# Optimization experiments

Hardware: AMD Instinct MI355X
Metric: run time of the kernel (lower is better)

The kernel has to match this reference:

```python
import jax, jax.numpy as jnp
import numpy as np
from jax import lax

DN = ('NCHW', 'OIHW', 'NCHW')

def conv3x3(x, w):
    return lax.conv_general_dilated(x, w, (1, 1), 'SAME', dimension_numbers=DN)

def conv1x1(x, w, b):
    # w: [O, C], x: [B, C, H, W]
    return jnp.einsum('oc,bchw->bohw', w, x) + b[None, :, None, None]

def bn_relu(x, p):
    # p: [2, C] -> (scale, shift), eval-mode folded BatchNorm + ReLU
    return jax.nn.relu(x * p[0][None, :, None, None] + p[1][None, :, None, None])

def pam(y, Wb, bb, Wc, bc, Wd, bd, alpha):
    B, C, H, W = y.shape
    n = H * W
    b_ = conv1x1(y, Wb, bb).reshape(B, -1, n)   # [B, C/8, N]
    c_ = conv1x1(y, Wc, bc).reshape(B, -1, n)   # [B, C/8, N]
    d_ = conv1x1(y, Wd, bd).reshape(B, C, n)    # [B, C, N]
    energy = jnp.einsum('bkn,bkm->bnm', b_, c_)  # [B, N, N]
    attn = jax.nn.softmax(energy, axis=-1)
    feat = jnp.einsum('bcm,bnm->bcn', d_, attn).reshape(B, C, H, W)
    return alpha[0] * feat + y

def cam(y, beta):
    B, C, H, W = y.shape
    xf = y.reshape(B, C, H * W)
    energy = jnp.einsum('bcn,bdn->bcd', xf, xf)  # [B, C, C]
    energy = jnp.max(energy, axis=-1, keepdims=True) - energy
    attn = jax.nn.softmax(energy, axis=-1)
    feat = jnp.einsum('bcd,bdn->bcn', attn, xf).reshape(B, C, H, W)
    return beta[0] * feat + y

def reference(x, Wp1, bnp1, Wc1, bnc1, Wb, bb, Wc, bc, Wd, bd, alpha, beta,
              Wp2, bnp2, Wc2, bnc2, Wout, bout, Wp3, bp3, Wc3, bc3):
    feat_p = bn_relu(conv3x3(x, Wp1), bnp1)
    feat_p = pam(feat_p, Wb, bb, Wc, bc, Wd, bd, alpha)
    feat_p = bn_relu(conv3x3(feat_p, Wp2), bnp2)

    feat_c = bn_relu(conv3x3(x, Wc1), bnc1)
    feat_c = cam(feat_c, beta)
    feat_c = bn_relu(conv3x3(feat_c, Wc2), bnc2)

    fusion = feat_p + feat_c
    out_main = jax.nn.sigmoid(conv1x1(fusion, Wout, bout))
    out_p = jax.nn.sigmoid(conv1x1(feat_p, Wp3, bp3))
    out_c = jax.nn.sigmoid(conv1x1(feat_c, Wc3, bc3))
    return (out_main, out_p, out_c)

def setup_inputs() -> dict:
    key = jax.random.key(0)
    ks = jax.random.split(key, 24)
    Cin, Ci, Ck, NC = 512, 128, 16, 19
    B, H, W = 8, 64, 64
    s = lambda k, shape, scale=0.05: jax.random.normal(k, shape, jnp.float32) * scale
    return {
        'x': jax.random.normal(ks[0], (B, Cin, H, W), jnp.float32),
        'Wp1': s(ks[1], (Ci, Cin, 3, 3)), 'bnp1': jnp.stack([jnp.ones(Ci), jnp.zeros(Ci)]),
        'Wc1': s(ks[2], (Ci, Cin, 3, 3)), 'bnc1': jnp.stack([jnp.ones(Ci), jnp.zeros(Ci)]),
        'Wb': s(ks[3], (Ck, Ci)), 'bb': s(ks[4], (Ck,)),
        'Wc': s(ks[5], (Ck, Ci)), 'bc': s(ks[6], (Ck,)),
        'Wd': s(ks[7], (Ci, Ci)), 'bd': s(ks[8], (Ci,)),
        'alpha': jax.random.normal(ks[9], (1,), jnp.float32) * 0.5,
        'beta': jax.random.normal(ks[10], (1,), jnp.float32) * 0.5,
        'Wp2': s(ks[11], (Ci, Ci, 3, 3)), 'bnp2': jnp.stack([jnp.ones(Ci), jnp.zeros(Ci)]),
        'Wc2': s(ks[12], (Ci, Ci, 3, 3)), 'bnc2': jnp.stack([jnp.ones(Ci), jnp.zeros(Ci)]),
        'Wout': s(ks[13], (NC, Ci)), 'bout': s(ks[14], (NC,)),
        'Wp3': s(ks[15], (NC, Ci)), 'bp3': s(ks[16], (NC,)),
        'Wc3': s(ks[17], (NC, Ci)), 'bc3': s(ks[18], (NC,)),
    }
```

## Files before the change

### kernel.cpp

```cpp
#include <hip/hip_runtime.h>
#include <math.h>


typedef __attribute__((ext_vector_type(8)))  short short8;
typedef __attribute__((ext_vector_type(16))) float f32x16;

__device__ inline unsigned short f2bf(float f) {
    union { float f; unsigned u; } v; v.f = f;
    unsigned r = v.u + 0x7fffu + ((v.u >> 16) & 1u);
    return (unsigned short)(r >> 16);
}
__device__ inline float bf2f(unsigned short h) {
    union { unsigned u; float f; } v; v.u = ((unsigned)h) << 16;
    return v.f;
}

__global__ __launch_bounds__(256) void wpack_kernel(
    const float* __restrict__ W, unsigned short* __restrict__ wp, int Cin, int total)
{
    int idx = blockIdx.x * 256 + threadIdx.x;
    if (idx >= total) return;
    int chunk = idx / 18432;
    int rem   = idx - chunk * 18432;
    int tap   = rem >> 11;
    int rem2  = rem & 2047;
    int co    = rem2 >> 4;
    int ci    = rem2 & 15;
    int cin   = (chunk << 4) + ci;
    wp[idx] = f2bf(W[((size_t)co * Cin + cin) * 9 + tap]);
}

__global__ __launch_bounds__(256) void wpack_split_kernel(
    const float* __restrict__ W, unsigned short* __restrict__ wph,
    unsigned short* __restrict__ wpl, int Cin, int total)
{
    int idx = blockIdx.x * 256 + threadIdx.x;
    if (idx >= total) return;
    int chunk = idx / 18432;
    int rem   = idx - chunk * 18432;
    int tap   = rem >> 11;
    int rem2  = rem & 2047;
    int co    = rem2 >> 4;
    int ci    = rem2 & 15;
    int cin   = (chunk << 4) + ci;
    float w = W[((size_t)co * Cin + cin) * 9 + tap];
    unsigned short hi = f2bf(w);
    wph[idx] = hi;
    wpl[idx] = f2bf(w - bf2f(hi));
}

__global__ __launch_bounds__(256) void x_split_kernel(
    const float* __restrict__ x, unsigned short* __restrict__ xh,
    unsigned short* __restrict__ xl)
{
    const int ch = blockIdx.x;
    const int b  = blockIdx.y;
    const int t  = threadIdx.x;
    for (int seg = 0; seg < 16; ++seg) {
        const int n = (seg << 8) + t;
        unsigned short uh[16], ul[16];
#pragma unroll
        for (int c = 0; c < 16; ++c) {
            float f = x[(((size_t)b * 512 + (ch << 4) + c) << 12) + n];
            unsigned short hi = f2bf(f);
            uh[c] = hi;
            ul[c] = f2bf(f - bf2f(hi));
        }
        size_t dst = ((((size_t)b * 32 + ch) << 12) + n) << 4;
        *(uint4*)(xh + dst)     = ((uint4*)uh)[0];
        *(uint4*)(xh + dst + 8) = ((uint4*)uh)[1];
        *(uint4*)(xl + dst)     = ((uint4*)ul)[0];
        *(uint4*)(xl + dst + 8) = ((uint4*)ul)[1];
    }
}

__global__ __launch_bounds__(256) void conv3x3_mfma(
    const unsigned short* __restrict__ xb, int Cin,
    const unsigned short* __restrict__ wpack, const float* __restrict__ bn,
    float* __restrict__ out_f32)
{
    const int t   = threadIdx.x;
    const int w   = t >> 6;
    const int wy  = w >> 1;
    const int wx  = w & 1;
    const int ln  = t & 63;
    const int l31 = ln & 31;
    const int g   = ln >> 5;
    const int y0  = blockIdx.x << 1;
    const int co0 = blockIdx.y << 6;
    const int b   = blockIdx.z;
    const int nc16 = Cin >> 4;

    __shared__ __align__(16) unsigned short Xl[4 * 66 * 16];
    __shared__ __align__(16) unsigned short Wl[9 * 64 * 16];

    if (t < 8) {
        int r = t >> 1, xc = (t & 1) * 65;
        uint4 z = {0, 0, 0, 0};
        *(uint4*)&Xl[(r * 66 + xc) * 16 + 0] = z;
        *(uint4*)&Xl[(r * 66 + xc) * 16 + 8] = z;
    }

    const f32x16 zero = {0,0,0,0,0,0,0,0,0,0,0,0,0,0,0,0};
    f32x16 acc0 = zero, acc1 = zero;

    for (int ch = 0; ch < nc16; ++ch) {
#pragma unroll
        for (int it = 0; it < 2; ++it) {
            int idx = t + (it << 8);
            int r = idx >> 7, u = idx & 127;
            int gy = y0 - 1 + r;
            uint4 val = {0, 0, 0, 0};
            if ((unsigned)gy < 64u)
                val = *(const uint4*)(xb + ((((size_t)(b * nc16 + ch)) << 12) + (gy << 6)) * 16 + (u << 3));
            *(uint4*)&Xl[(r * 66 + 1) * 16 + (u << 3)] = val;
        }
        {
            const uint4* wsrc = (const uint4*)wpack;
            const int base = ch * 2304 + (co0 << 1);
            for (int idx = t; idx < 1152; idx += 256)
                ((uint4*)Wl)[idx] = wsrc[base + ((idx >> 7) << 8) + (idx & 127)];
        }
        __syncthreads();

#pragma unroll 3
        for (int tap = 0; tap < 9; ++tap) {
            const int dy = tap / 3, dx = tap - dy * 3;
            short8 a = *(const short8*)&Wl[((tap << 6) + (wy << 5) + l31) * 16 + (g << 3)];
            const int row = wx + dy;
            short8 b0 = *(const short8*)&Xl[(row * 66 + l31 + dx) * 16 + (g << 3)];
            short8 b1 = *(const short8*)&Xl[(row * 66 + l31 + 32 + dx) * 16 + (g << 3)];
            acc0 = __builtin_amdgcn_mfma_f32_32x32x16_bf16(a, b0, acc0, 0, 0, 0);
            acc1 = __builtin_amdgcn_mfma_f32_32x32x16_bf16(a, b1, acc1, 0, 0, 0);
        }
        __syncthreads();
    }

    const int y = y0 + wx;
#pragma unroll
    for (int j = 0; j < 2; j++) {
        const f32x16 a = j ? acc1 : acc0;
#pragma unroll
        for (int r = 0; r < 16; r++) {
            int co = co0 + (wy << 5) + (r & 3) + ((r >> 2) << 3) + (g << 2);
            int x  = (j << 5) + l31;
            float v = fmaf(a[r], bn[co], bn[128 + co]);
            v = v > 0.f ? v : 0.f;
            out_f32[(((size_t)b * 128 + co) << 12) + (y << 6) + x] = v;
        }
    }
}

__global__ __launch_bounds__(256) void conv3x3_mfma_hilo(
    const unsigned short* __restrict__ xbh, const unsigned short* __restrict__ xbl,
    int Cin, const unsigned short* __restrict__ wph, const unsigned short* __restrict__ wpl,
    const float* __restrict__ bn, float* __restrict__ out_f32,
    unsigned short* __restrict__ outh, unsigned short* __restrict__ outl)
{
    const int t   = threadIdx.x;
    const int w   = t >> 6;
    const int wy  = w >> 1;
    const int wx  = w & 1;
    const int ln  = t & 63;
    const int l31 = ln & 31;
    const int g   = ln >> 5;
    const int y0  = blockIdx.x << 1;
    const int co0 = blockIdx.y << 6;
    const int b   = blockIdx.z;
    const int nc16 = Cin >> 4;

    __shared__ __align__(16) unsigned short Xh[4 * 66 * 16];
    __shared__ __align__(16) unsigned short Xo[4 * 66 * 16];
    __shared__ __align__(16) unsigned short Wh[9 * 64 * 16];
    __shared__ __align__(16) unsigned short Wo[9 * 64 * 16];

    if (t < 8) {
        int r = t >> 1, xc = (t & 1) * 65;
        uint4 z = {0, 0, 0, 0};
        *(uint4*)&Xh[(r * 66 + xc) * 16 + 0] = z;
        *(uint4*)&Xh[(r * 66 + xc) * 16 + 8] = z;
        *(uint4*)&Xo[(r * 66 + xc) * 16 + 0] = z;
        *(uint4*)&Xo[(r * 66 + xc) * 16 + 8] = z;
    }

    const f32x16 zero = {0,0,0,0,0,0,0,0,0,0,0,0,0,0,0,0};
    f32x16 acc0 = zero, acc1 = zero;

    for (int ch = 0; ch < nc16; ++ch) {
#pragma unroll
        for (int it = 0; it < 2; ++it) {
            int idx = t + (it << 8);
            int r = idx >> 7, u = idx & 127;
            int gy = y0 - 1 + r;
            uint4 vh = {0, 0, 0, 0}, vl = {0, 0, 0, 0};
            if ((unsigned)gy < 64u) {
                size_t o = ((((size_t)(b * nc16 + ch)) << 12) + (gy << 6)) * 16 + (u << 3);
                vh = *(const uint4*)(xbh + o);
                vl = *(const uint4*)(xbl + o);
            }
            *(uint4*)&Xh[(r * 66 + 1) * 16 + (u << 3)] = vh;
            *(uint4*)&Xo[(r * 66 + 1) * 16 + (u << 3)] = vl;
        }
        {
            const uint4* sh = (const uint4*)wph;
            const uint4* sl = (const uint4*)wpl;
            const int base = ch * 2304 + (co0 << 1);
            for (int idx = t; idx < 1152; idx += 256) {
                int o = base + ((idx >> 7) << 8) + (idx & 127);
                ((uint4*)Wh)[idx] = sh[o];
                ((uint4*)Wo)[idx] = sl[o];
            }
        }
        __syncthreads();

#pragma unroll 1
        for (int tap = 0; tap < 9; ++tap) {
            const int dy = tap / 3, dx = tap - dy * 3;
            const int wi = ((tap << 6) + (wy << 5) + l31) * 16 + (g << 3);
            const int row = wx + dy;
            const int xi0 = (row * 66 + l31 + dx) * 16 + (g << 3);
            const int xi1 = (row * 66 + l31 + 32 + dx) * 16 + (g << 3);
            short8 ah = *(const short8*)&Wh[wi];
            short8 al = *(const short8*)&Wo[wi];
            short8 b0h = *(const short8*)&Xh[xi0];
            short8 b1h = *(const short8*)&Xh[xi1];
            short8 b0l = *(const short8*)&Xo[xi0];
            short8 b1l = *(const short8*)&Xo[xi1];
            acc0 = __builtin_amdgcn_mfma_f32_32x32x16_bf16(ah, b0h, acc0, 0, 0, 0);
            acc1 = __builtin_amdgcn_mfma_f32_32x32x16_bf16(ah, b1h, acc1, 0, 0, 0);
            acc0 = __builtin_amdgcn_mfma_f32_32x32x16_bf16(ah, b0l, acc0, 0, 0, 0);
            acc1 = __builtin_amdgcn_mfma_f32_32x32x16_bf16(ah, b1l, acc1, 0, 0, 0);
            acc0 = __builtin_amdgcn_mfma_f32_32x32x16_bf16(al, b0h, acc0, 0, 0, 0);
            acc1 = __builtin_amdgcn_mfma_f32_32x32x16_bf16(al, b1h, acc1, 0, 0, 0);
        }
        __syncthreads();
    }

    const int y = y0 + wx;
#pragma unroll
    for (int j = 0; j < 2; j++) {
        const f32x16 a = j ? acc1 : acc0;
#pragma unroll
        for (int r = 0; r < 16; r++) {
            int co = co0 + (wy << 5) + (r & 3) + ((r >> 2) << 3) + (g << 2);
            int x  = (j << 5) + l31;
            float v = fmaf(a[r], bn[co], bn[128 + co]);
            v = v > 0.f ? v : 0.f;
            size_t o = (((size_t)b * 128 + co) << 12) + (y << 6) + x;
            if (out_f32) out_f32[o] = v;
            if (outh) {
                unsigned short hi = f2bf(v);
                outh[o] = hi;
                outl[o] = f2bf(v - bf2f(hi));
            }
        }
    }
}

__global__ __launch_bounds__(256) void cam_energy_mfma(
    const unsigned short* __restrict__ bh, const unsigned short* __restrict__ bl,
    float* __restrict__ egy_part)
{
    const int t   = threadIdx.x;
    const int w   = t >> 6;
    const int ln  = t & 63;
    const int l31 = ln & 31;
    const int g   = ln >> 5;
    const int i0  = (blockIdx.x >> 2) << 5;
    const int j0  = (blockIdx.x & 3) << 5;
    const int nseg = blockIdx.y;
    const int b   = blockIdx.z;

    __shared__ float red[4][64][17];

    const f32x16 zero = {0,0,0,0,0,0,0,0,0,0,0,0,0,0,0,0};
    f32x16 acc = zero;
    const int nb = (nseg << 9) + (w << 7) + (g << 3);
    const size_t ri = ((size_t)b * 128 + i0 + l31) << 12;
    const size_t rj = ((size_t)b * 128 + j0 + l31) << 12;

#pragma unroll
    for (int c = 0; c < 8; c++) {
        const int n0 = nb + (c << 4);
        short8 ah  = *(const short8*)(bh + ri + n0);
        short8 al  = *(const short8*)(bl + ri + n0);
        short8 bhf = *(const short8*)(bh + rj + n0);
        short8 blf = *(const short8*)(bl + rj + n0);
        acc = __builtin_amdgcn_mfma_f32_32x32x16_bf16(ah, bhf, acc, 0, 0, 0);
        acc = __builtin_amdgcn_mfma_f32_32x32x16_bf16(ah, blf, acc, 0, 0, 0);
        acc = __builtin_amdgcn_mfma_f32_32x32x16_bf16(al, bhf, acc, 0, 0, 0);
    }
#pragma unroll
    for (int r = 0; r < 16; r++) red[w][ln][r] = acc[r];
    __syncthreads();

    const int lane = t & 63;
    const int rq   = t >> 6;
    float* base = egy_part + (((size_t)(nseg * 8 + b)) << 14);
#pragma unroll
    for (int e = 0; e < 4; e++) {
        const int reg = (rq << 2) + e;
        float v = red[0][lane][reg] + red[1][lane][reg]
                + red[2][lane][reg] + red[3][lane][reg];
        const int i = i0 + (reg & 3) + ((reg >> 2) << 3) + ((lane >> 5) << 2);
        base[i * 128 + j0 + (lane & 31)] = v;
    }
}

__global__ __launch_bounds__(256) void cam_softmax_fused(
    const float* __restrict__ egy_part, float* __restrict__ egy)
{
    const int b   = blockIdx.x;
    const int rg  = blockIdx.y;
    const int t   = threadIdx.x;
    const int row = (rg << 4) + (t >> 4);
    const int jg  = t & 15;

    float e[8];
#pragma unroll
    for (int jj = 0; jj < 8; jj++) e[jj] = 0.f;
    for (int seg = 0; seg < 8; seg++) {
        const float* p = egy_part + (((size_t)(seg * 8 + b)) << 14) + row * 128 + (jg << 3);
#pragma unroll
        for (int jj = 0; jj < 8; jj++) e[jj] += p[jj];
    }
    float mn = e[0];
#pragma unroll
    for (int jj = 1; jj < 8; jj++) mn = fminf(mn, e[jj]);
#pragma unroll
    for (int k = 1; k < 16; k <<= 1) mn = fminf(mn, __shfl_xor(mn, k));
    float s = 0.f;
#pragma unroll
    for (int jj = 0; jj < 8; jj++) { float p = __expf(mn - e[jj]); e[jj] = p; s += p; }
#pragma unroll
    for (int k = 1; k < 16; k <<= 1) s += __shfl_xor(s, k);
    const float inv = 1.f / s;
    float* orow = egy + ((size_t)b << 14) + row * 128 + (jg << 3);
#pragma unroll
    for (int jj = 0; jj < 8; jj++) orow[jj] = e[jj] * inv;
}

__global__ __launch_bounds__(256) void pam_qk_1x1(
    const float* __restrict__ A, const float* __restrict__ Wb, const float* __restrict__ bb,
    const float* __restrict__ Wc, const float* __restrict__ bc,
    unsigned short* __restrict__ qt, unsigned short* __restrict__ kt)
{
    __shared__ float wl[2 * 16 * 128];
    __shared__ float bl[32];
    const int t = threadIdx.x;
    const int n = (blockIdx.x << 8) + t;
    const int b = blockIdx.y;
    for (int idx = t; idx < 2048; idx += 256) { wl[idx] = Wb[idx]; wl[2048 + idx] = Wc[idx]; }
    if (t < 16) { bl[t] = bb[t]; bl[16 + t] = bc[t]; }
    __syncthreads();
    float ab[16], ac[16];
#pragma unroll
    for (int k = 0; k < 16; k++) { ab[k] = 0.f; ac[k] = 0.f; }
    for (int chn = 0; chn < 128; ++chn) {
        float a = A[(((size_t)b * 128 + chn) << 12) + n];
#pragma unroll
        for (int k = 0; k < 16; k++) {
            ab[k] = fmaf(wl[k * 128 + chn], a, ab[k]);
            ac[k] = fmaf(wl[2048 + k * 128 + chn], a, ac[k]);
        }
    }
    unsigned short uq[16], uk[16];
#pragma unroll
    for (int k = 0; k < 16; k++) {
        uq[k] = f2bf(ab[k] + bl[k]);
        uk[k] = f2bf(ac[k] + bl[16 + k]);
    }
    size_t row = (size_t)b * 4096 + n;
    ((uint4*)qt)[row * 2 + 0] = ((uint4*)uq)[0];
    ((uint4*)qt)[row * 2 + 1] = ((uint4*)uq)[1];
    ((uint4*)kt)[row * 2 + 0] = ((uint4*)uk)[0];
    ((uint4*)kt)[row * 2 + 1] = ((uint4*)uk)[1];
}

__global__ __launch_bounds__(256) void pam_v_1x1(
    const float* __restrict__ A, const float* __restrict__ Wd, const float* __restrict__ bd,
    unsigned short* __restrict__ vbB)
{
    __shared__ float wl[32 * 128];
    __shared__ float bl[32];
    const int t   = threadIdx.x;
    const int n   = (blockIdx.x << 8) + t;
    const int co0 = blockIdx.y << 5;
    const int b   = blockIdx.z;
    for (int idx = t; idx < 4096; idx += 256) {
        int c2 = idx >> 7, chv = idx & 127;
        wl[idx] = Wd[(co0 + c2) * 128 + chv];
    }
    if (t < 32) bl[t] = bd[co0 + t];
    __syncthreads();
    float acc[32];
#pragma unroll
    for (int k = 0; k < 32; k++) acc[k] = 0.f;
    for (int chn = 0; chn < 128; ++chn) {
        float a = A[(((size_t)b * 128 + chn) << 12) + n];
#pragma unroll
        for (int k = 0; k < 32; k++) acc[k] = fmaf(wl[k * 128 + chn], a, acc[k]);
    }
    const size_t mbase = (((size_t)b * 256 + (n >> 4)) * 128 + co0) * 16 + (n & 15);
#pragma unroll
    for (int k = 0; k < 32; k++)
        vbB[mbase + (size_t)k * 16] = f2bf(acc[k] + bl[k]);
}

__global__ __launch_bounds__(256) void pam_rowmax(
    const unsigned short* __restrict__ qt, const unsigned short* __restrict__ kt,
    float* __restrict__ rowmax)
{
    const int t  = threadIdx.x;
    const int w  = t >> 6;
    const int L  = t & 63;
    const int ln = L & 31;
    const int g  = L >> 5;
    const int b  = blockIdx.y;
    const int n0 = blockIdx.x << 5;
    __shared__ float red[4][32];

    const f32x16 zero = {0,0,0,0,0,0,0,0,0,0,0,0,0,0,0,0};
    short8 qfrag = *(const short8*)(qt + (((size_t)b * 4096 + n0 + ln) << 4) + (g << 3));

    float mx = -INFINITY;
    for (int mq = (w << 5); mq < 4096; mq += 128) {
        short8 kfrag = *(const short8*)(kt + (((size_t)b * 4096 + mq + ln) << 4) + (g << 3));
        f32x16 s = __builtin_amdgcn_mfma_f32_32x32x16_bf16(kfrag, qfrag, zero, 0, 0, 0);
#pragma unroll
        for (int r = 0; r < 16; r++) mx = fmaxf(mx, s[r]);
    }
    mx = fmaxf(mx, __shfl_xor(mx, 32));
    if (L < 32) red[w][L] = mx;
    __syncthreads();
    if (t < 32) {
        float m = fmaxf(fmaxf(red[0][t], red[1][t]), fmaxf(red[2][t], red[3][t]));
        rowmax[((size_t)b << 12) + n0 + t] = m;
    }
}

__global__ __launch_bounds__(256) void pam_attn_mfma(
    const unsigned short* __restrict__ qt, const unsigned short* __restrict__ kt,
    const unsigned short* __restrict__ vbB, const float* __restrict__ rowmax,
    float* __restrict__ part, float* __restrict__ lsum)
{
    const int t  = threadIdx.x;
    const int w  = t >> 6;
    const int L  = t & 63;
    const int ln = L & 31;
    const int g  = L >> 5;
    const int mh = blockIdx.y;
    const int b  = blockIdx.z;
    const int n0 = blockIdx.x << 5;
    const int c0 = w << 5;

    __shared__ unsigned short Pf[16 * 256];
    __shared__ float red[4][32];

    const f32x16 zero = {0,0,0,0,0,0,0,0,0,0,0,0,0,0,0,0};
    short8 qfrag = *(const short8*)(qt + (((size_t)b * 4096 + n0 + ln) << 4) + (g << 3));
    const float rm = rowmax[((size_t)b << 12) + n0 + ln];

    f32x16 acc = zero;
    float rs = 0.f;

    const int mbeg = mh << 11;
    for (int m0 = mbeg; m0 < mbeg + 2048; m0 += 128) {
        const int mq = m0 + (w << 5);
        short8 kfrag = *(const short8*)(kt + (((size_t)b * 4096 + mq + ln) << 4) + (g << 3));
        f32x16 s = __builtin_amdgcn_mfma_f32_32x32x16_bf16(kfrag, qfrag, zero, 0, 0, 0);

        float p[16];
#pragma unroll
        for (int r = 0; r < 16; r++) { p[r] = __expf(s[r] - rm); rs += p[r]; }
        float xx[16];
#pragma unroll
        for (int r = 0; r < 16; r++) xx[r] = __shfl_xor(p[r], 32);

        unsigned short f0[8], f1[8];
#pragma unroll
        for (int i = 0; i < 4; i++) {
            f0[i]     = f2bf(g ? xx[4 + i]  : p[i]);
            f0[4 + i] = f2bf(g ? p[4 + i]   : xx[i]);
            f1[i]     = f2bf(g ? xx[12 + i] : p[8 + i]);
            f1[4 + i] = f2bf(g ? p[12 + i]  : xx[8 + i]);
        }
        *(short8*)(&Pf[((w << 2) + g) * 256 + (ln << 3)])     = *(short8*)f0;
        *(short8*)(&Pf[((w << 2) + 2 + g) * 256 + (ln << 3)]) = *(short8*)f1;
        __syncthreads();

        const int mc0 = m0 >> 4;
#pragma unroll
        for (int kk = 0; kk < 8; kk++) {
            short8 pfrag = *(const short8*)(&Pf[((kk << 1) + g) * 256 + (ln << 3)]);
            short8 vfrag = *(const short8*)(vbB + (((size_t)b * 256 + mc0 + kk) * 128
                                                    + c0 + ln) * 16 + (g << 3));
            acc = __builtin_amdgcn_mfma_f32_32x32x16_bf16(vfrag, pfrag, acc, 0, 0, 0);
        }
        __syncthreads();
    }

    rs += __shfl_xor(rs, 32);
    if (L < 32) red[w][L] = rs;
    __syncthreads();
    if (t < 32)
        lsum[(((size_t)(mh * 8 + b)) << 12) + n0 + t]
            = red[0][t] + red[1][t] + red[2][t] + red[3][t];

    const int n = n0 + ln;
#pragma unroll
    for (int r = 0; r < 16; r++) {
        int c = c0 + (r & 3) + ((r >> 2) << 3) + (g << 2);
        part[((((size_t)(mh * 8 + b)) * 128 + c) << 12) + n] = acc[r];
    }
}

__global__ __launch_bounds__(256) void pam_combine(
    const float* __restrict__ part, const float* __restrict__ lsum,
    const float* __restrict__ alpha, const float* __restrict__ Y,
    unsigned short* __restrict__ outb)
{
    const int t = threadIdx.x;
    const int n = (blockIdx.x << 8) + t;
    const int b = blockIdx.y;
    const size_t h1 = (size_t)8 * 128 * 4096;
    const float l = lsum[((size_t)b << 12) + n] + lsum[(((size_t)(8 + b)) << 12) + n];
    const float sc = alpha[0] / l;
#pragma unroll 1
    for (int cg = 0; cg < 8; ++cg) {
        unsigned short o[16];
#pragma unroll
        for (int j = 0; j < 16; ++j) {
            const int c = (cg << 4) + j;
            const size_t idx = (((size_t)b * 128 + c) << 12) + n;
            float v = fmaf(sc, part[idx] + part[h1 + idx], Y[idx]);
            o[j] = f2bf(v);
        }
        size_t dst = ((((size_t)b * 8 + cg) << 12) + n) << 4;
        *(uint4*)(outb + dst)     = ((uint4*)o)[0];
        *(uint4*)(outb + dst + 8) = ((uint4*)o)[1];
    }
}

__global__ __launch_bounds__(256) void cam_feat(
    const float* __restrict__ attn, const unsigned short* __restrict__ bh,
    const unsigned short* __restrict__ blo, const float* __restrict__ beta,
    unsigned short* __restrict__ camh, unsigned short* __restrict__ caml)
{
    const int t  = threadIdx.x;
    const int n  = (blockIdx.x << 8) + t;
    const int c0 = blockIdx.y << 5;
    const int b  = blockIdx.z;
    __shared__ float al[32 * 128];
    for (int idx = t; idx < 4096; idx += 256)
        al[idx] = attn[((size_t)b << 14) + (c0 + (idx >> 7)) * 128 + (idx & 127)];
    __syncthreads();
    float acc[32];
#pragma unroll
    for (int k = 0; k < 32; k++) acc[k] = 0.f;
    for (int d = 0; d < 128; ++d) {
        size_t idx = (((size_t)b * 128 + d) << 12) + n;
        float v = bf2f(bh[idx]) + bf2f(blo[idx]);
#pragma unroll
        for (int k = 0; k < 32; k++) acc[k] = fmaf(al[k * 128 + d], v, acc[k]);
    }
    float be = beta[0];
    unsigned short oh[32], ol[32];
#pragma unroll
    for (int k = 0; k < 32; k++) {
        size_t idx = (((size_t)b * 128 + c0 + k) << 12) + n;
        float bfv = bf2f(bh[idx]) + bf2f(blo[idx]);
        float v = fmaf(be, acc[k], bfv);
        unsigned short hi = f2bf(v);
        oh[k] = hi;
        ol[k] = f2bf(v - bf2f(hi));
    }
    const int g0 = c0 >> 4;
    size_t d0 = ((((size_t)b * 8 + g0) << 12) + n) << 4;
    size_t d1 = ((((size_t)b * 8 + g0 + 1) << 12) + n) << 4;
    *(uint4*)(camh + d0)     = ((uint4*)oh)[0];
    *(uint4*)(camh + d0 + 8) = ((uint4*)oh)[1];
    *(uint4*)(camh + d1)     = ((uint4*)oh)[2];
    *(uint4*)(camh + d1 + 8) = ((uint4*)oh)[3];
    *(uint4*)(caml + d0)     = ((uint4*)ol)[0];
    *(uint4*)(caml + d0 + 8) = ((uint4*)ol)[1];
    *(uint4*)(caml + d1)     = ((uint4*)ol)[2];
    *(uint4*)(caml + d1 + 8) = ((uint4*)ol)[3];
}

__global__ __launch_bounds__(256) void heads(
    const float* __restrict__ FP, const float* __restrict__ FC,
    const float* __restrict__ Wout, const float* __restrict__ bout,
    const float* __restrict__ Wp3, const float* __restrict__ bp3,
    const float* __restrict__ Wc3, const float* __restrict__ bc3,
    float* __restrict__ out)
{
    const int t = threadIdx.x;
    const int n = (blockIdx.x << 8) + t;
    const int b = blockIdx.y;
    __shared__ float wl[3 * 19 * 128];
    __shared__ float bl[3 * 19];
    for (int idx = t; idx < 2432; idx += 256) {
        wl[idx]        = Wout[idx];
        wl[2432 + idx] = Wp3[idx];
        wl[4864 + idx] = Wc3[idx];
    }
    if (t < 19) { bl[t] = bout[t]; bl[19 + t] = bp3[t]; bl[38 + t] = bc3[t]; }
    __syncthreads();
    float am[19], ap[19], ac[19];
#pragma unroll
    for (int o = 0; o < 19; o++) { am[o] = 0.f; ap[o] = 0.f; ac[o] = 0.f; }
    for (int chn = 0; chn < 128; ++chn) {
        float pv = FP[(((size_t)b * 128 + chn) << 12) + n];
        float cv = FC[(((size_t)b * 128 + chn) << 12) + n];
        float fv = pv + cv;
#pragma unroll
        for (int o = 0; o < 19; o++) {
            am[o] = fmaf(wl[o * 128 + chn], fv, am[o]);
            ap[o] = fmaf(wl[2432 + o * 128 + chn], pv, ap[o]);
            ac[o] = fmaf(wl[4864 + o * 128 + chn], cv, ac[o]);
        }
    }
    const size_t OS = (size_t)8 * 19 * 4096;
#pragma unroll
    for (int o = 0; o < 19; o++) {
        size_t base = (((size_t)b * 19 + o) << 12) + n;
        out[base]          = 1.f / (1.f + __expf(-(am[o] + bl[o])));
        out[OS + base]     = 1.f / (1.f + __expf(-(ap[o] + bl[19 + o])));
        out[2 * OS + base] = 1.f / (1.f + __expf(-(ac[o] + bl[38 + o])));
    }
}

extern "C" void kernel_launch(void* const* d_in, const int* in_sizes, int n_in,
                              void* d_out, int out_size, void* d_ws, size_t ws_size,
                              hipStream_t stream)
{
    const float* x     = (const float*)d_in[0];
    const float* Wp1   = (const float*)d_in[1];
    const float* bnp1  = (const float*)d_in[2];
    const float* Wc1   = (const float*)d_in[3];
    const float* bnc1  = (const float*)d_in[4];
    const float* Wb    = (const float*)d_in[5];
    const float* bb    = (const float*)d_in[6];
    const float* Wc    = (const float*)d_in[7];
    const float* bcv   = (const float*)d_in[8];
    const float* Wd    = (const float*)d_in[9];
    const float* bd    = (const float*)d_in[10];
    const float* alpha = (const float*)d_in[11];
    const float* beta  = (const float*)d_in[12];
    const float* Wp2   = (const float*)d_in[13];
    const float* bnp2  = (const float*)d_in[14];
    const float* Wc2   = (const float*)d_in[15];
    const float* bnc2  = (const float*)d_in[16];
    const float* Wout  = (const float*)d_in[17];
    const float* bo    = (const float*)d_in[18];
    const float* Wp3   = (const float*)d_in[19];
    const float* bp3   = (const float*)d_in[20];
    const float* Wc3   = (const float*)d_in[21];
    const float* bc3   = (const float*)d_in[22];
    float* out = (float*)d_out;

    char* ws = (char*)d_ws;
    const size_t MB = 1u << 20;
    const size_t W1SZ = (size_t)32 * 18432 * 2;
    const size_t W2SZ = (size_t)8 * 18432 * 2;
    float*          bufA     = (float*)(ws);
    unsigned short* bh       = (unsigned short*)(ws + 16 * MB);
    unsigned short* blo      = (unsigned short*)(ws + 24 * MB);
    unsigned short* xh       = (unsigned short*)(ws + 32 * MB);
    unsigned short* xl       = (unsigned short*)(ws + 64 * MB);
    float*          egy_part = (float*)(ws + 32 * MB);
    unsigned short* qt       = (unsigned short*)(ws + 36 * MB);
    unsigned short* kt       = (unsigned short*)(ws + 37 * MB);
    float*          rowmax   = (float*)(ws + 38 * MB);
    float*          egy      = (float*)(ws + 38 * MB + (1u << 17));
    unsigned short* vbB      = (unsigned short*)(ws + 39 * MB);
    float*          part     = (float*)(ws + 47 * MB);
    float*          lsum     = (float*)(ws + 79 * MB);
    unsigned short* pam_bfB  = (unsigned short*)(ws + 80 * MB);
    float*          bufD     = (float*)(ws + 47 * MB);
    unsigned short* camh     = (unsigned short*)(ws + 63 * MB);
    unsigned short* caml     = (unsigned short*)(ws + 71 * MB);
    unsigned short* wp1      = (unsigned short*)(ws + 96 * MB);
    unsigned short* wc1h     = (unsigned short*)(ws + 96 * MB + W1SZ);
    unsigned short* wc1l     = (unsigned short*)(ws + 96 * MB + 2 * W1SZ);
    unsigned short* wp2      = (unsigned short*)(ws + 96 * MB + 3 * W1SZ);
    unsigned short* wc2h     = (unsigned short*)(ws + 96 * MB + 3 * W1SZ + W2SZ);
    unsigned short* wc2l     = (unsigned short*)(ws + 96 * MB + 3 * W1SZ + 2 * W2SZ);

    dim3 blk(256);
    const int n1 = 32 * 18432;
    const int n2 = 8 * 18432;
    wpack_kernel<<<dim3((n1 + 255) / 256), blk, 0, stream>>>(Wp1, wp1, 512, n1);
    wpack_kernel<<<dim3((n2 + 255) / 256), blk, 0, stream>>>(Wp2, wp2, 128, n2);
    wpack_split_kernel<<<dim3((n1 + 255) / 256), blk, 0, stream>>>(Wc1, wc1h, wc1l, 512, n1);
    wpack_split_kernel<<<dim3((n2 + 255) / 256), blk, 0, stream>>>(Wc2, wc2h, wc2l, 128, n2);

    x_split_kernel<<<dim3(32, 8), blk, 0, stream>>>(x, xh, xl);

    conv3x3_mfma<<<dim3(32, 2, 8), blk, 0, stream>>>(xh, 512, wp1, bnp1, bufA);
    conv3x3_mfma_hilo<<<dim3(32, 2, 8), blk, 0, stream>>>(xh, xl, 512, wc1h, wc1l, bnc1,
                                                          (float*)0, bh, blo);
    cam_energy_mfma<<<dim3(16, 8, 8), blk, 0, stream>>>(bh, blo, egy_part);
    cam_softmax_fused<<<dim3(8, 8), blk, 0, stream>>>(egy_part, egy);

    pam_qk_1x1<<<dim3(16, 8), blk, 0, stream>>>(bufA, Wb, bb, Wc, bcv, qt, kt);
    pam_v_1x1<<<dim3(16, 4, 8), blk, 0, stream>>>(bufA, Wd, bd, vbB);
    pam_rowmax<<<dim3(128, 8), blk, 0, stream>>>(qt, kt, rowmax);
    pam_attn_mfma<<<dim3(128, 2, 8), blk, 0, stream>>>(qt, kt, vbB, rowmax, part, lsum);
    pam_combine<<<dim3(16, 8), blk, 0, stream>>>(part, lsum, alpha, bufA, pam_bfB);

    conv3x3_mfma<<<dim3(32, 2, 8), blk, 0, stream>>>(pam_bfB, 128, wp2, bnp2, bufD);

    cam_feat<<<dim3(16, 4, 8), blk, 0, stream>>>(egy, bh, blo, beta, camh, caml);
    conv3x3_mfma_hilo<<<dim3(32, 2, 8), blk, 0, stream>>>(camh, caml, 128, wc2h, wc2l, bnc2,
                                                          bufA, (unsigned short*)0, (unsigned short*)0);

    heads<<<dim3(16, 8), blk, 0, stream>>>(bufD, bufA, Wout, bo, Wp3, bp3, Wc3, bc3, out);
}
```

Baseline: 866.2 us.

## Retile 3x3 convs to 8-row blocks with split-K atomic accumulation and separate BN combine

The conv kernels now have each block cover 8 output rows and all 64 output channels, with 8 accumulators per wave so each weight fragment is reused across more pixels. The input-channel loop is split across blocks (Ksplit 4 or 2), and partial sums are added into zeroed fp32 buffers with atomicAdd. A separate combine kernel then applies BN+ReLU and the hi/lo bf16 split. The aim is more MFMA reuse per LDS load while keeping enough blocks in flight. The cost is extra memsets, float atomics, extra global round trips, a reshuffled workspace layout and nondeterministic summation order.

Measured after the change: 972.8 us. 1.12x slower.

```diff
diff --git a/kernel.cpp b/kernel.cpp
--- a/kernel.cpp
+++ b/kernel.cpp
@@ -74,40 +74,43 @@
     }
 }
 
-__global__ __launch_bounds__(256) void conv3x3_mfma(
-    const unsigned short* __restrict__ xb, int Cin,
-    const unsigned short* __restrict__ wpack, const float* __restrict__ bn,
-    float* __restrict__ out_f32)
+__global__ __launch_bounds__(256) void conv3x3_plain_part(
+    const unsigned short* __restrict__ xb, int nc16, int Ksplit,
+    const unsigned short* __restrict__ wpack, float* __restrict__ accb)
 {
     const int t   = threadIdx.x;
     const int w   = t >> 6;
-    const int wy  = w >> 1;
-    const int wx  = w & 1;
     const int ln  = t & 63;
     const int l31 = ln & 31;
     const int g   = ln >> 5;
-    const int y0  = blockIdx.x << 1;
+    const int y0  = blockIdx.x << 3;
     const int co0 = blockIdx.y << 6;
-    const int b   = blockIdx.z;
-    const int nc16 = Cin >> 4;
-
-    __shared__ __align__(16) unsigned short Xl[4 * 66 * 16];
+    const int b   = blockIdx.z / Ksplit;
+    const int ks  = blockIdx.z % Ksplit;
+    const int cps = nc16 / Ksplit;
+    const int ch0 = ks * cps;
+
+    __shared__ __align__(16) unsigned short Xl[10 * 66 * 16];
     __shared__ __align__(16) unsigned short Wl[9 * 64 * 16];
 
-    if (t < 8) {
-        int r = t >> 1, xc = (t & 1) * 65;
+    if (t < 20) {
+        int r = t >> 1, col = (t & 1) * 65;
         uint4 z = {0, 0, 0, 0};
-        *(uint4*)&Xl[(r * 66 + xc) * 16 + 0] = z;
-        *(uint4*)&Xl[(r * 66 + xc) * 16 + 8] = z;
+        *(uint4*)&Xl[(r * 66 + col) * 16 + 0] = z;
+        *(uint4*)&Xl[(r * 66 + col) * 16 + 8] = z;
     }
 
     const f32x16 zero = {0,0,0,0,0,0,0,0,0,0,0,0,0,0,0,0};
-    f32x16 acc0 = zero, acc1 = zero;
-
-    for (int ch = 0; ch < nc16; ++ch) {
-#pragma unroll
-        for (int it = 0; it < 2; ++it) {
-            int idx = t + (it << 8);
+    f32x16 acc[2][2][2];
+#pragma unroll
+    for (int i = 0; i < 2; i++)
+#pragma unroll
+        for (int r = 0; r < 2; r++)
+#pragma unroll
+            for (int j = 0; j < 2; j++) acc[i][r][j] = zero;
+
+    for (int ch = ch0; ch < ch0 + cps; ++ch) {
+        for (int idx = t; idx < 1280; idx += 256) {
             int r = idx >> 7, u = idx & 127;
             int gy = y0 - 1 + r;
             uint4 val = {0, 0, 0, 0};
@@ -123,73 +126,86 @@
         }
         __syncthreads();
 
-#pragma unroll 3
+#pragma unroll 1
         for (int tap = 0; tap < 9; ++tap) {
             const int dy = tap / 3, dx = tap - dy * 3;
-            short8 a = *(const short8*)&Wl[((tap << 6) + (wy << 5) + l31) * 16 + (g << 3)];
-            const int row = wx + dy;
-            short8 b0 = *(const short8*)&Xl[(row * 66 + l31 + dx) * 16 + (g << 3)];
-            short8 b1 = *(const short8*)&Xl[(row * 66 + l31 + 32 + dx) * 16 + (g << 3)];
-            acc0 = __builtin_amdgcn_mfma_f32_32x32x16_bf16(a, b0, acc0, 0, 0, 0);
-            acc1 = __builtin_amdgcn_mfma_f32_32x32x16_bf16(a, b1, acc1, 0, 0, 0);
+            short8 a0 = *(const short8*)&Wl[((tap << 6) + l31) * 16 + (g << 3)];
+            short8 a1 = *(const short8*)&Wl[((tap << 6) + 32 + l31) * 16 + (g << 3)];
+#pragma unroll
+            for (int r = 0; r < 2; ++r) {
+                const int row = (w << 1) + r + dy;
+                short8 b0 = *(const short8*)&Xl[(row * 66 + l31 + dx) * 16 + (g << 3)];
+                short8 b1 = *(const short8*)&Xl[(row * 66 + l31 + 32 + dx) * 16 + (g << 3)];
+                acc[0][r][0] = __builtin_amdgcn_mfma_f32_32x32x16_bf16(a0, b0, acc[0][r][0], 0, 0, 0);
+                acc[0][r][1] = __builtin_amdgcn_mfma_f32_32x32x16_bf16(a0, b1, acc[0][r][1], 0, 0, 0);
+                acc[1][r][0] = __builtin_amdgcn_mfma_f32_32x32x16_bf16(a1, b0, acc[1][r][0], 0, 0, 0);
+                acc[1][r][1] = __builtin_amdgcn_mfma_f32_32x32x16_bf16(a1, b1, acc[1][r][1], 0, 0, 0);
+            }
         }
         __syncthreads();
     }
 
-    const int y = y0 + wx;
-#pragma unroll
-    for (int j = 0; j < 2; j++) {
-        const f32x16 a = j ? acc1 : acc0;
-#pragma unroll
-        for (int r = 0; r < 16; r++) {
-            int co = co0 + (wy << 5) + (r & 3) + ((r >> 2) << 3) + (g << 2);
-            int x  = (j << 5) + l31;
-            float v = fmaf(a[r], bn[co], bn[128 + co]);
-            v = v > 0.f ? v : 0.f;
-            out_f32[(((size_t)b * 128 + co) << 12) + (y << 6) + x] = v;
-        }
-    }
-}
-
-__global__ __launch_bounds__(256) void conv3x3_mfma_hilo(
+#pragma unroll
+    for (int i = 0; i < 2; i++)
+#pragma unroll
+        for (int r = 0; r < 2; r++) {
+            const int y = y0 + (w << 1) + r;
+#pragma unroll
+            for (int j = 0; j < 2; j++) {
+                const int x = (j << 5) + l31;
+#pragma unroll
+                for (int reg = 0; reg < 16; reg++) {
+                    int co = co0 + (i << 5) + (reg & 3) + ((reg >> 2) << 3) + (g << 2);
+                    atomicAdd(&accb[(((size_t)b * 128 + co) << 12) + (y << 6) + x],
+                              acc[i][r][j][reg]);
+                }
+            }
+        }
+}
+
+__global__ __launch_bounds__(256) void conv3x3_hilo_part(
     const unsigned short* __restrict__ xbh, const unsigned short* __restrict__ xbl,
-    int Cin, const unsigned short* __restrict__ wph, const unsigned short* __restrict__ wpl,
-    const float* __restrict__ bn, float* __restrict__ out_f32,
-    unsigned short* __restrict__ outh, unsigned short* __restrict__ outl)
+    int nc16, int Ksplit,
+    const unsigned short* __restrict__ wph, const unsigned short* __restrict__ wpl,
+    float* __restrict__ accb)
 {
     const int t   = threadIdx.x;
     const int w   = t >> 6;
-    const int wy  = w >> 1;
-    const int wx  = w & 1;
     const int ln  = t & 63;
     const int l31 = ln & 31;
     const int g   = ln >> 5;
-    const int y0  = blockIdx.x << 1;
+    const int y0  = blockIdx.x << 3;
     const int co0 = blockIdx.y << 6;
-    const int b   = blockIdx.z;
-    const int nc16 = Cin >> 4;
-
-    __shared__ __align__(16) unsigned short Xh[4 * 66 * 16];
-    __shared__ __align__(16) unsigned short Xo[4 * 66 * 16];
+    const int b   = blockIdx.z / Ksplit;
+    const int ks  = blockIdx.z % Ksplit;
+    const int cps = nc16 / Ksplit;
+    const int ch0 = ks * cps;
+
+    __shared__ __align__(16) unsigned short Xh[10 * 66 * 16];
+    __shared__ __align__(16) unsigned short Xo[10 * 66 * 16];
     __shared__ __align__(16) unsigned short Wh[9 * 64 * 16];
     __shared__ __align__(16) unsigned short Wo[9 * 64 * 16];
 
-    if (t < 8) {
-        int r = t >> 1, xc = (t & 1) * 65;
+    if (t < 20) {
+        int r = t >> 1, col = (t & 1) * 65;
         uint4 z = {0, 0, 0, 0};
-        *(uint4*)&Xh[(r * 66 + xc) * 16 + 0] = z;
-        *(uint4*)&Xh[(r * 66 + xc) * 16 + 8] = z;
-        *(uint4*)&Xo[(r * 66 + xc) * 16 + 0] = z;
-        *(uint4*)&Xo[(r * 66 + xc) * 16 + 8] = z;
+        *(uint4*)&Xh[(r * 66 + col) * 16 + 0] = z;
+        *(uint4*)&Xh[(r * 66 + col) * 16 + 8] = z;
+        *(uint4*)&Xo[(r * 66 + col) * 16 + 0] = z;
+        *(uint4*)&Xo[(r * 66 + col) * 16 + 8] = z;
     }
 
     const f32x16 zero = {0,0,0,0,0,0,0,0,0,0,0,0,0,0,0,0};
-    f32x16 acc0 = zero, acc1 = zero;
-
-    for (int ch = 0; ch < nc16; ++ch) {
-#pragma unroll
-        for (int it = 0; it < 2; ++it) {
-            int idx = t + (it << 8);
+    f32x16 acc[2][2][2];
+#pragma unroll
+    for (int i = 0; i < 2; i++)
+#pragma unroll
+        for (int r = 0; r < 2; r++)
+#pragma unroll
+            for (int j = 0; j < 2; j++) acc[i][r][j] = zero;
+
+    for (int ch = ch0; ch < ch0 + cps; ++ch) {
+        for (int idx = t; idx < 1280; idx += 256) {
             int r = idx >> 7, u = idx & 127;
             int gy = y0 - 1 + r;
             uint4 vh = {0, 0, 0, 0}, vl = {0, 0, 0, 0};
@@ -216,44 +232,78 @@
 #pragma unroll 1
         for (int tap = 0; tap < 9; ++tap) {
             const int dy = tap / 3, dx = tap - dy * 3;
-            const int wi = ((tap << 6) + (wy << 5) + l31) * 16 + (g << 3);
-            const int row = wx + dy;
-            const int xi0 = (row * 66 + l31 + dx) * 16 + (g << 3);
-            const int xi1 = (row * 66 + l31 + 32 + dx) * 16 + (g << 3);
-            short8 ah = *(const short8*)&Wh[wi];
-            short8 al = *(const short8*)&Wo[wi];
-            short8 b0h = *(const short8*)&Xh[xi0];
-            short8 b1h = *(const short8*)&Xh[xi1];
-            short8 b0l = *(const short8*)&Xo[xi0];
-            short8 b1l = *(const short8*)&Xo[xi1];
-            acc0 = __builtin_amdgcn_mfma_f32_32x32x16_bf16(ah, b0h, acc0, 0, 0, 0);
-            acc1 = __builtin_amdgcn_mfma_f32_32x32x16_bf16(ah, b1h, acc1, 0, 0, 0);
-            acc0 = __builtin_amdgcn_mfma_f32_32x32x16_bf16(ah, b0l, acc0, 0, 0, 0);
-            acc1 = __builtin_amdgcn_mfma_f32_32x32x16_bf16(ah, b1l, acc1, 0, 0, 0);
-            acc0 = __builtin_amdgcn_mfma_f32_32x32x16_bf16(al, b0h, acc0, 0, 0, 0);
-            acc1 = __builtin_amdgcn_mfma_f32_32x32x16_bf16(al, b1h, acc1, 0, 0, 0);
+            short8 ah0 = *(const short8*)&Wh[((tap << 6) + l31) * 16 + (g << 3)];
+            short8 ah1 = *(const short8*)&Wh[((tap << 6) + 32 + l31) * 16 + (g << 3)];
+            short8 al0 = *(const short8*)&Wo[((tap << 6) + l31) * 16 + (g << 3)];
+            short8 al1 = *(const short8*)&Wo[((tap << 6) + 32 + l31) * 16 + (g << 3)];
+#pragma unroll
+            for (int r = 0; r < 2; ++r) {
+                const int row = (w << 1) + r + dy;
+#pragma unroll
+                for (int j = 0; j < 2; ++j) {
+                    const int xi = (row * 66 + l31 + (j << 5) + dx) * 16 + (g << 3);
+                    short8 bhf = *(const short8*)&Xh[xi];
+                    short8 blf = *(const short8*)&Xo[xi];
+                    acc[0][r][j] = __builtin_amdgcn_mfma_f32_32x32x16_bf16(ah0, bhf, acc[0][r][j], 0, 0, 0);
+                    acc[1][r][j] = __builtin_amdgcn_mfma_f32_32x32x16_bf16(ah1, bhf, acc[1][r][j], 0, 0, 0);
+                    acc[0][r][j] = __builtin_amdgcn_mfma_f32_32x32x16_bf16(ah0, blf, acc[0][r][j], 0, 0, 0);
+                    acc[1][r][j] = __builtin_amdgcn_mfma_f32_32x32x16_bf16(ah1, blf, acc[1][r][j], 0, 0, 0);
+                    acc[0][r][j] = __builtin_amdgcn_mfma_f32_32x32x16_bf16(al0, bhf, acc[0][r][j], 0, 0, 0);
+                    acc[1][r][j] = __builtin_amdgcn_mfma_f32_32x32x16_bf16(al1, bhf, acc[1][r][j], 0, 0, 0);
+                }
+            }
         }
         __syncthreads();
     }
 
-    const int y = y0 + wx;
-#pragma unroll
-    for (int j = 0; j < 2; j++) {
-        const f32x16 a = j ? acc1 : acc0;
-#pragma unroll
-        for (int r = 0; r < 16; r++) {
-            int co = co0 + (wy << 5) + (r & 3) + ((r >> 2) << 3) + (g << 2);
-            int x  = (j << 5) + l31;
-            float v = fmaf(a[r], bn[co], bn[128 + co]);
-            v = v > 0.f ? v : 0.f;
-            size_t o = (((size_t)b * 128 + co) << 12) + (y << 6) + x;
-            if (out_f32) out_f32[o] = v;
-            if (outh) {
-                unsigned short hi = f2bf(v);
-                outh[o] = hi;
-                outl[o] = f2bf(v - bf2f(hi));
+#pragma unroll
+    for (int i = 0; i < 2; i++)
+#pragma unroll
+        for (int r = 0; r < 2; r++) {
+            const int y = y0 + (w << 1) + r;
+#pragma unroll
+            for (int j = 0; j < 2; j++) {
+                const int x = (j << 5) + l31;
+#pragma unroll
+                for (int reg = 0; reg < 16; reg++) {
+                    int co = co0 + (i << 5) + (reg & 3) + ((reg >> 2) << 3) + (g << 2);
+                    atomicAdd(&accb[(((size_t)b * 128 + co) << 12) + (y << 6) + x],
+                              acc[i][r][j][reg]);
+                }
             }
         }
+}
+
+__global__ __launch_bounds__(256) void combine_plain(
+    const float* __restrict__ acc, const float* __restrict__ bn,
+    float* __restrict__ outf)
+{
+    const int t = threadIdx.x;
+    const int n = (blockIdx.x << 8) + t;
+    const int b = blockIdx.y;
+#pragma unroll 4
+    for (int co = 0; co < 128; ++co) {
+        size_t idx = (((size_t)b * 128 + co) << 12) + n;
+        float v = fmaf(acc[idx], bn[co], bn[128 + co]);
+        outf[idx] = v > 0.f ? v : 0.f;
+    }
+}
+
+__global__ __launch_bounds__(256) void combine_hilo(
+    const float* __restrict__ acc, const float* __restrict__ bn,
+    unsigned short* __restrict__ bh, unsigned short* __restrict__ blo)
+{
+    const int t = threadIdx.x;
+    const int n = (blockIdx.x << 8) + t;
+    const int b = blockIdx.y;
+#pragma unroll 4
+    for (int co = 0; co < 128; ++co) {
+        size_t idx = (((size_t)b * 128 + co) << 12) + n;
+        float v = fmaf(acc[idx], bn[co], bn[128 + co]);
+        v = v > 0.f ? v : 0.f;
+        unsigned short hi = f2bf(v);
+        bh[idx]  = hi;
+        blo[idx] = f2bf(v - bf2f(hi));
     }
 }
 
@@ -662,25 +712,30 @@
 
     char* ws = (char*)d_ws;
     const size_t MB = 1u << 20;
+    const size_t KB = 1u << 10;
     const size_t W1SZ = (size_t)32 * 18432 * 2;
     const size_t W2SZ = (size_t)8 * 18432 * 2;
-    float*          bufA     = (float*)(ws);
+    float*          acc1     = (float*)(ws);
     unsigned short* bh       = (unsigned short*)(ws + 16 * MB);
     unsigned short* blo      = (unsigned short*)(ws + 24 * MB);
     unsigned short* xh       = (unsigned short*)(ws + 32 * MB);
     unsigned short* xl       = (unsigned short*)(ws + 64 * MB);
-    float*          egy_part = (float*)(ws + 32 * MB);
-    unsigned short* qt       = (unsigned short*)(ws + 36 * MB);
-    unsigned short* kt       = (unsigned short*)(ws + 37 * MB);
-    float*          rowmax   = (float*)(ws + 38 * MB);
-    float*          egy      = (float*)(ws + 38 * MB + (1u << 17));
-    unsigned short* vbB      = (unsigned short*)(ws + 39 * MB);
-    float*          part     = (float*)(ws + 47 * MB);
-    float*          lsum     = (float*)(ws + 79 * MB);
-    unsigned short* pam_bfB  = (unsigned short*)(ws + 80 * MB);
-    float*          bufD     = (float*)(ws + 47 * MB);
-    unsigned short* camh     = (unsigned short*)(ws + 63 * MB);
-    unsigned short* caml     = (unsigned short*)(ws + 71 * MB);
+    float*          bufA     = (float*)(ws + 64 * MB);
+    float*          egy_part = (float*)(ws + 80 * MB);
+    float*          egy      = (float*)(ws + 84 * MB);
+    float*          rowmax   = (float*)(ws + 84 * MB + 512 * KB);
+    float*          lsum     = (float*)(ws + 84 * MB + 640 * KB);
+    unsigned short* qt       = (unsigned short*)(ws + 85 * MB);
+    unsigned short* kt       = (unsigned short*)(ws + 86 * MB);
+    unsigned short* vbB      = (unsigned short*)(ws + 88 * MB);
+    float*          part     = (float*)(ws + 32 * MB);
+    unsigned short* pam_bfB  = (unsigned short*)(ws);
+    float*          acc2     = (float*)(ws + 32 * MB);
+    float*          bufD     = (float*)(ws + 48 * MB);
+    unsigned short* camh     = (unsigned short*)(ws);
+    unsigned short* caml     = (unsigned short*)(ws + 8 * MB);
+    float*          acc3     = (float*)(ws + 16 * MB);
+    float*          bufC     = (float*)(ws + 64 * MB);
     unsigned short* wp1      = (unsigned short*)(ws + 96 * MB);
     unsigned short* wc1h     = (unsigned short*)(ws + 96 * MB + W1SZ);
     unsigned short* wc1l     = (unsigned short*)(ws + 96 * MB + 2 * W1SZ);
@@ -698,9 +753,13 @@
 
     x_split_kernel<<<dim3(32, 8), blk, 0, stream>>>(x, xh, xl);
 
-    conv3x3_mfma<<<dim3(32, 2, 8), blk, 0, stream>>>(xh, 512, wp1, bnp1, bufA);
-    conv3x3_mfma_hilo<<<dim3(32, 2, 8), blk, 0, stream>>>(xh, xl, 512, wc1h, wc1l, bnc1,
-                                                          (float*)0, bh, blo);
+    hipMemsetAsync(acc1, 0, 16 * MB, stream);
+    conv3x3_hilo_part<<<dim3(8, 2, 32), blk, 0, stream>>>(xh, xl, 32, 4, wc1h, wc1l, acc1);
+    combine_hilo<<<dim3(16, 8), blk, 0, stream>>>(acc1, bnc1, bh, blo);
+    hipMemsetAsync(acc1, 0, 16 * MB, stream);
+    conv3x3_plain_part<<<dim3(8, 2, 32), blk, 0, stream>>>(xh, 32, 4, wp1, acc1);
+    combine_plain<<<dim3(16, 8), blk, 0, stream>>>(acc1, bnp1, bufA);
+
     cam_energy_mfma<<<dim3(16, 8, 8), blk, 0, stream>>>(bh, blo, egy_part);
     cam_softmax_fused<<<dim3(8, 8), blk, 0, stream>>>(egy_part, egy);
 
@@ -710,11 +769,14 @@
     pam_attn_mfma<<<dim3(128, 2, 8), blk, 0, stream>>>(qt, kt, vbB, rowmax, part, lsum);
     pam_combine<<<dim3(16, 8), blk, 0, stream>>>(part, lsum, alpha, bufA, pam_bfB);
 
-    conv3x3_mfma<<<dim3(32, 2, 8), blk, 0, stream>>>(pam_bfB, 128, wp2, bnp2, bufD);
+    hipMemsetAsync(acc2, 0, 16 * MB, stream);
+    conv3x3_plain_part<<<dim3(8, 2, 16), blk, 0, stream>>>(pam_bfB, 8, 2, wp2, acc2);
+    combine_plain<<<dim3(16, 8), blk, 0, stream>>>(acc2, bnp2, bufD);
 
     cam_feat<<<dim3(16, 4, 8), blk, 0, stream>>>(egy, bh, blo, beta, camh, caml);
-    conv3x3_mfma_hilo<<<dim3(32, 2, 8), blk, 0, stream>>>(camh, caml, 128, wc2h, wc2l, bnc2,
-                                                          bufA, (unsigned short*)0, (unsigned short*)0);
-
-    heads<<<dim3(16, 8), blk, 0, stream>>>(bufD, bufA, Wout, bo, Wp3, bp3, Wc3, bc3, out);
-}
+    hipMemsetAsync(acc3, 0, 16 * MB, stream);
+    conv3x3_hilo_part<<<dim3(8, 2, 16), blk, 0, stream>>>(camh, caml, 8, 2, wc2h, wc2l, acc3);
+    combine_plain<<<dim3(16, 8), blk, 0, stream>>>(acc3, bnc2, bufC);
+
+    heads<<<dim3(16, 8), blk, 0, stream>>>(bufD, bufC, Wout, bo, Wp3, bp3, Wc3, bc3, out);
+}
```
